# Kernel optimization log

Measured on AMD Instinct MI355X. Metric: run time of the kernel, lower is better.

## Reference

```python
import jax, jax.numpy as jnp
import numpy as np

N = 20000        # nodes
E = 320000       # edges (avg degree 16)
F_IN = 128       # node_features
F2 = 64          # second_features (per-head out dim, LSTM hidden)
H = 8            # heads
D1 = H * F2      # 512, concat output of GATConv / LSTM input
NEG_SLOPE = 0.2  # GATConv default leaky_relu slope


def _gat_conv(x, src, dst, W, att_src, att_dst, bias):
    """PyG GATConv (concat=True, self-loops added, eval-mode dropout)."""
    n = x.shape[0]
    h = (x @ W).reshape(n, H, -1)                      # [N,H,F]
    a_s = (h * att_src).sum(-1)                        # [N,H]
    a_d = (h * att_dst).sum(-1)                        # [N,H]
    e = jax.nn.leaky_relu(a_s[src] + a_d[dst], NEG_SLOPE)   # [E',H]
    m = jax.ops.segment_max(e, dst, num_segments=n)    # [N,H]
    m = jnp.where(jnp.isfinite(m), m, 0.0)
    ex = jnp.exp(e - m[dst])
    denom = jax.ops.segment_sum(ex, dst, num_segments=n)
    alpha = ex / (denom[dst] + 1e-16)                  # [E',H]
    msg = h[src] * alpha[:, :, None]                   # [E',H,F]
    out = jax.ops.segment_sum(msg, dst, num_segments=n)  # [N,H,F]
    return out.reshape(n, -1) + bias                   # [N,H*F]


def _lstm_step(x, W_ih, W_hh, b_ih, b_hh):
    """Single-timestep PyTorch LSTM with zero initial (h0, c0). x: [N,D1]."""
    h0 = jnp.zeros((x.shape[0], F2), x.dtype)
    gates = x @ W_ih.T + b_ih + h0 @ W_hh.T + b_hh     # [N,4*F2]
    i, f, g, o = jnp.split(gates, 4, axis=-1)
    c = jax.nn.sigmoid(f) * 0.0 + jax.nn.sigmoid(i) * jnp.tanh(g)
    h = jax.nn.sigmoid(o) * jnp.tanh(c)
    return h, (h, c)


def setup_inputs() -> dict:
    key = jax.random.key(0)
    ks = jax.random.split(key, 16)

    def glorot(k, shape, fan_in):
        return jax.random.normal(k, shape, jnp.float32) * (1.0 / np.sqrt(fan_in))

    return {
        "x": jax.random.normal(ks[0], (N, F_IN), jnp.float32),
        "edge_index": jax.random.randint(ks[1], (2, E), 0, N, jnp.int32),
        "edge_weight": jax.random.uniform(ks[2], (E,), jnp.float32),
        # GATConv 1: F_IN -> H*F2
        "W1": glorot(ks[3], (F_IN, H * F2), F_IN),
        "att_src1": glorot(ks[4], (H, F2), F2),
        "att_dst1": glorot(ks[5], (H, F2), F2),
        "bias1": jnp.zeros((H * F2,), jnp.float32),
        # LSTM: input D1 -> hidden F2
        "W_ih": glorot(ks[6], (4 * F2, D1), D1),
        "W_hh": glorot(ks[7], (4 * F2, F2), F2),
        "b_ih": jnp.zeros((4 * F2,), jnp.float32),
        "b_hh": jnp.zeros((4 * F2,), jnp.float32),
        # GATConv 2: F2 -> H*F2
        "W2": glorot(ks[8], (F2, H * F2), F2),
        "att_src2": glorot(ks[9], (H, F2), F2),
        "att_dst2": glorot(ks[10], (H, F2), F2),
        "bias2": jnp.zeros((H * F2,), jnp.float32),
    }


def reference(x, edge_index, edge_weight, W1, att_src1, att_dst1, bias1,
              W_ih, W_hh, b_ih, b_hh, W2, att_src2, att_dst2, bias2):
    # edge_weight is accepted but unused, matching the original forward.
    loops = jnp.arange(N, dtype=edge_index.dtype)
    src = jnp.concatenate([edge_index[0], loops])      # add self-loops (PyG default)
    dst = jnp.concatenate([edge_index[1], loops])

    h = _gat_conv(x, src, dst, W1, att_src1, att_dst1, bias1)   # [N,512]
    h, hidden2 = _lstm_step(h, W_ih, W_hh, b_ih, b_hh)          # [N,64]
    h = jax.nn.relu(h)
    h = _gat_conv(h, src, dst, W2, att_src2, att_dst2, bias2)   # [N,512]
    return jax.nn.softmax(h, axis=1)
```

## Files before the change

kernel.cpp:

```cpp
#include <hip/hip_runtime.h>
#include <math.h>
#include <stdint.h>


__global__ void count_kernel(const int* __restrict__ dst, int* __restrict__ deg, int E) {
  int i = blockIdx.x * 256 + threadIdx.x;
  if (i < E) atomicAdd(&deg[dst[i]], 1);
}

__global__ void scan_kernel(const int* __restrict__ deg, int* __restrict__ rowptr, int n) {
  __shared__ int buf[1024];
  const int tid = threadIdx.x;
  const int i0 = tid * 20;
  int v[20];
  int tsum = 0;
#pragma unroll
  for (int k = 0; k < 20; ++k) {
    int i = i0 + k;
    v[k] = (i < n) ? (deg[i] + 1) : 0;
    tsum += v[k];
  }
  int incl = tsum;
  buf[tid] = incl;
  __syncthreads();
  for (int s = 1; s < 1024; s <<= 1) {
    int t = (tid >= (unsigned)s) ? buf[tid - s] : 0;
    __syncthreads();
    incl += t;
    buf[tid] = incl;
    __syncthreads();
  }
  int excl = incl - tsum;
#pragma unroll
  for (int k = 0; k < 20; ++k) {
    int i = i0 + k;
    if (i < n) rowptr[i] = excl;
    excl += v[k];
  }
  if (tid == 1023) rowptr[n] = incl;
}

__global__ void scatter_kernel(const int* __restrict__ src, const int* __restrict__ dst,
                               const int* __restrict__ rowptr, int* __restrict__ wp,
                               int* __restrict__ col, int E, int n) {
  int i = blockIdx.x * 256 + threadIdx.x;
  if (i < E) {
    int d = dst[i];
    int p = rowptr[d] + atomicAdd(&wp[d], 1);
    col[p] = src[i];
  } else if (i < E + n) {
    int d = i - E;
    int p = rowptr[d] + atomicAdd(&wp[d], 1);
    col[p] = d;
  }
}


__device__ __forceinline__ uint16_t bf16r(float x) {
  uint32_t u = __float_as_uint(x);
  return (uint16_t)((u + 0x7FFFu + ((u >> 16) & 1u)) >> 16);
}
__device__ __forceinline__ void bfsplit(float x, uint16_t& h, uint16_t& l) {
  h = bf16r(x);
  float hf = __uint_as_float((uint32_t)h << 16);
  l = bf16r(x - hf);
}
__device__ __forceinline__ void store4split(uint16_t* oh, uint16_t* ol, float4 v) {
  ushort4 h, l;
  bfsplit(v.x, h.x, l.x); bfsplit(v.y, h.y, l.y);
  bfsplit(v.z, h.z, l.z); bfsplit(v.w, h.w, l.w);
  *reinterpret_cast<ushort4*>(oh) = h;
  *reinterpret_cast<ushort4*>(ol) = l;
}

__device__ __forceinline__ void gload16(const uint16_t* g, uint16_t* l) {
  __builtin_amdgcn_global_load_lds(
      (const __attribute__((address_space(1))) uint32_t*)g,
      (__attribute__((address_space(3))) uint32_t*)l, 16, 0, 0);
}

using bf16x8 = __attribute__((ext_vector_type(8))) short;
using f32x4  = __attribute__((ext_vector_type(4))) float;


template <bool SPLIT_OUT>
__global__ __launch_bounds__(256) void gemm_mfma(
    const uint16_t* __restrict__ Ah, const uint16_t* __restrict__ Al,
    const uint16_t* __restrict__ Bh, const uint16_t* __restrict__ Bl,
    float* __restrict__ C, uint16_t* __restrict__ Ch, uint16_t* __restrict__ Cl,
    const float* __restrict__ bias,
    int M, int K, int lda, int aZ, int bZ, int ldc, int cZ, int biasZ) {
  constexpr int BM = 64, BN = 64, BK = 64;
  constexpr int PL = BM * BK;
  __shared__ __align__(16) uint16_t sAh[2 * PL], sAl[2 * PL];
  __shared__ __align__(16) uint16_t sBh[2 * PL], sBl[2 * PL];
  const int z = blockIdx.z;
  Ah += (size_t)z * aZ; Al += (size_t)z * aZ;
  Bh += (size_t)z * bZ; Bl += (size_t)z * bZ;
  const int tid = threadIdx.x;
  const int wid = tid >> 6, lane = tid & 63;
  int L = blockIdx.x + gridDim.x * blockIdx.y;
  int nwg = gridDim.x * gridDim.y;
  int q = nwg >> 3, r = nwg & 7;
  int xcd = L & 7, gix = L >> 3;
  int base = (xcd < r) ? xcd * (q + 1) : r * (q + 1) + (xcd - r) * q;
  int w = base + gix;
  const int bm = (w / gridDim.x) * BM;
  const int bn = (w % gridDim.x) * BN;
  const int fr = lane & 15;
  const int kg = lane >> 4;
  const int mbase = wid * 16;
  f32x4 acc[4] = {};

  auto stage = [&](int sb, int k0) {
#pragma unroll
    for (int j = 0; j < 2; ++j) {
      int idx = (wid * 2 + j) * 64 + lane;
      int row = idx >> 3, c = idx & 7;
      int rg = min(bm + row, M - 1);
      size_t goA = (size_t)rg * lda + k0 + ((c ^ (row & 7)) << 3);
      uint16_t* ldst = sAh + sb * PL + (wid * 2 + j) * 512;
      gload16(Ah + goA, ldst);
      gload16(Al + goA, sAl + sb * PL + (wid * 2 + j) * 512);
      size_t goB = (size_t)(bn + row) * K + k0 + ((c ^ (row & 7)) << 3);
      gload16(Bh + goB, sBh + sb * PL + (wid * 2 + j) * 512);
      gload16(Bl + goB, sBl + sb * PL + (wid * 2 + j) * 512);
    }
  };

  stage(0, 0);
  __syncthreads();
  int buf = 0;
  for (int k0 = 0; k0 < K; k0 += BK) {
    const bool more = (k0 + BK) < K;
    if (more) stage(buf ^ 1, k0 + BK);
    const char* pAh = (const char*)sAh + buf * (PL * 2);
    const char* pAl = (const char*)sAl + buf * (PL * 2);
    const char* pBh = (const char*)sBh + buf * (PL * 2);
    const char* pBl = (const char*)sBl + buf * (PL * 2);
#pragma unroll
    for (int ks = 0; ks < 2; ++ks) {
      const int kc = ks * 4 + kg;
      bf16x8 ah, al, bh[4], bl[4];
      {
        int m = mbase + fr;
        int off = m * 128 + ((kc ^ (m & 7)) << 4);
        ah = *reinterpret_cast<const bf16x8*>(pAh + off);
        al = *reinterpret_cast<const bf16x8*>(pAl + off);
      }
#pragma unroll
      for (int j = 0; j < 4; ++j) {
        int n = j * 16 + fr;
        int off = n * 128 + ((kc ^ (n & 7)) << 4);
        bh[j] = *reinterpret_cast<const bf16x8*>(pBh + off);
        bl[j] = *reinterpret_cast<const bf16x8*>(pBl + off);
      }
#pragma unroll
      for (int j = 0; j < 4; ++j) {
        acc[j] = __builtin_amdgcn_mfma_f32_16x16x32_bf16(ah, bh[j], acc[j], 0, 0, 0);
        acc[j] = __builtin_amdgcn_mfma_f32_16x16x32_bf16(al, bh[j], acc[j], 0, 0, 0);
        acc[j] = __builtin_amdgcn_mfma_f32_16x16x32_bf16(ah, bl[j], acc[j], 0, 0, 0);
      }
    }
    if (more) {
      __syncthreads();
      buf ^= 1;
    }
  }
  float bz[4];
#pragma unroll
  for (int j = 0; j < 4; ++j)
    bz[j] = bias ? bias[(size_t)z * biasZ + bn + j * 16 + fr] : 0.f;
  if (SPLIT_OUT) {
    Ch += (size_t)z * cZ;
    Cl += (size_t)z * cZ;
  } else {
    C += (size_t)z * cZ;
  }
  {
    int mr = bm + mbase + kg * 4;
#pragma unroll
    for (int rr = 0; rr < 4; ++rr) {
      int m = mr + rr;
      if (m < M) {
#pragma unroll
        for (int j = 0; j < 4; ++j) {
          float v = acc[j][rr] + bz[j];
          size_t o = (size_t)m * ldc + bn + j * 16 + fr;
          if (SPLIT_OUT) {
            uint16_t h, l;
            bfsplit(v, h, l);
            Ch[o] = h; Cl[o] = l;
          } else {
            C[o] = v;
          }
        }
      }
    }
  }
}


__global__ void prep_all_kernel(const float* __restrict__ W_ih, const float* __restrict__ b_ih,
                                const float* __restrict__ b_hh, const float* __restrict__ W1,
                                const float* __restrict__ as1, const float* __restrict__ ad1,
                                const float* __restrict__ W2, const float* __restrict__ as2,
                                const float* __restrict__ ad2,
                                int* __restrict__ degwp,
                                uint16_t* __restrict__ Wtbh, uint16_t* __restrict__ Wtbl,
                                uint16_t* __restrict__ Bt1h, uint16_t* __restrict__ Bt1l,
                                uint16_t* __restrict__ Bt2h, uint16_t* __restrict__ Bt2l,
                                float* __restrict__ bsum, float* __restrict__ watt1,
                                float* __restrict__ watt2, int n2) {
  int idx = blockIdx.x * 256 + threadIdx.x;
  if (idx < n2) {
    degwp[idx] = 0;
    return;
  }
  int t = idx - n2;
  if (t < 98304) {
    int jp = t >> 9, k = t & 511;
    int j = (jp < 64) ? jp : jp + 64;
    uint16_t h, l;
    bfsplit(W_ih[(size_t)j * 512 + k], h, l);
    Wtbh[t] = h; Wtbl[t] = l;
    return;
  }
  t -= 98304;
  if (t < 65536) {
    int n = t >> 7, k = t & 127;
    uint16_t h, l;
    bfsplit(W1[(size_t)k * 512 + n], h, l);
    Bt1h[t] = h; Bt1l[t] = l;
    return;
  }
  t -= 65536;
  if (t < 32768) {
    int n = t >> 6, k = t & 63;
    uint16_t h, l;
    bfsplit(W2[(size_t)k * 512 + n], h, l);
    Bt2h[t] = h; Bt2l[t] = l;
    return;
  }
  t -= 32768;
  if (t < 192) {
    int j = (t < 64) ? t : t + 64;
    bsum[t] = b_ih[j] + b_hh[j];
    return;
  }
  t -= 192;
  if (t < 2048) {
    int f = t >> 4, c = t & 15;
    int k = c & 7;
    const float* att = ((c < 8) ? as1 : ad1) + k * 64;
    const float* w = W1 + (size_t)f * 512 + k * 64;
    float s = 0.f;
#pragma unroll
    for (int j = 0; j < 64; ++j) s = fmaf(w[j], att[j], s);
    watt1[t] = s;
    return;
  }
  t -= 2048;
  if (t < 1024) {
    int f = t >> 4, c = t & 15;
    int k = c & 7;
    const float* att = ((c < 8) ? as2 : ad2) + k * 64;
    const float* w = W2 + (size_t)f * 512 + k * 64;
    float s = 0.f;
#pragma unroll
    for (int j = 0; j < 64; ++j) s = fmaf(w[j], att[j], s);
    watt2[t] = s;
  }
}


template <int F>
__global__ __launch_bounds__(256) void attcoef_kernel(
    const float* __restrict__ feat, const float* __restrict__ watt,
    float* __restrict__ a_s, float* __restrict__ a_d, int n) {
  __shared__ float rows[16 * F];
  __shared__ float wbuf[F * 16];
  const int n0 = blockIdx.x * 16;
  const int tid = threadIdx.x;
  if (n0 + 16 <= n) {
    const float4* g = reinterpret_cast<const float4*>(feat + (size_t)n0 * F);
    float4* l = reinterpret_cast<float4*>(rows);
    for (int i = tid; i < 16 * F / 4; i += 256) l[i] = g[i];
  } else {
    for (int i = tid; i < 16 * F; i += 256) {
      int r = i / F;
      rows[i] = (n0 + r < n) ? feat[(size_t)(n0 + r) * F + (i - r * F)] : 0.f;
    }
  }
  {
    const float4* g = reinterpret_cast<const float4*>(watt);
    float4* l = reinterpret_cast<float4*>(wbuf);
    for (int i = tid; i < F * 16 / 4; i += 256) l[i] = g[i];
  }
  __syncthreads();
  const int local = tid >> 4, c = tid & 15;
  float s = 0.f;
#pragma unroll 8
  for (int f = 0; f < F; ++f) s = fmaf(rows[local * F + f], wbuf[f * 16 + c], s);
  const int node = n0 + local;
  if (node < n) {
    if (c < 8) a_s[(size_t)node * 8 + c] = s;
    else       a_d[(size_t)node * 8 + (c - 8)] = s;
  }
}


template <int F>
__global__ __launch_bounds__(256) void gat_aggregate_wave(
    const float* __restrict__ feat, const float* __restrict__ a_s,
    const float* __restrict__ a_d, const int* __restrict__ rowptr,
    const int* __restrict__ col, uint16_t* __restrict__ aggH,
    uint16_t* __restrict__ aggL, int n) {
  constexpr int FL = F / 4;
  constexpr int GROUPS = 64 / FL;
  constexpr int HPW = 8 / GROUPS;
  __shared__ float s_ex[4][8][8];
  __shared__ int s_cols[4][8];
  const int wid = threadIdx.x >> 6;
  const int lane = threadIdx.x & 63;
  const int node = blockIdx.x * 4 + wid;
  if (node >= n) return;
  const int start = rowptr[node];
  const int deg = rowptr[node + 1] - start;
  const int j = lane >> 3;
  const int h = lane & 7;
  const int grp = lane / FL;
  const int fl = lane % FL;
  const float adh = a_d[(size_t)node * 8 + h];
  float dpart = 0.f;
  float acc[8][4];
#pragma unroll
  for (int q = 0; q < 8; ++q)
#pragma unroll
    for (int t = 0; t < 4; ++t) acc[q][t] = 0.f;

  for (int c0 = 0; c0 < deg; c0 += 8) {
    float ex = 0.f;
    int sj = 0;
    if (c0 + j < deg) {
      sj = col[start + c0 + j];
      float v = a_s[(size_t)sj * 8 + h] + adh;
      v = (v > 0.f) ? v : 0.2f * v;
      ex = __expf(v);
    }
    s_ex[wid][j][h] = ex;
    if (h == 0) s_cols[wid][j] = sj;
    dpart += ex;
    __builtin_amdgcn_wave_barrier();
    const int ce = min(8, deg - c0);
    for (int e = grp; e < ce; e += GROUPS) {
      int s = s_cols[wid][e];
      float4 fv = *reinterpret_cast<const float4*>(feat + (size_t)s * F + fl * 4);
      float al[8];
      *reinterpret_cast<float4*>(&al[0]) = *reinterpret_cast<const float4*>(&s_ex[wid][e][0]);
      *reinterpret_cast<float4*>(&al[4]) = *reinterpret_cast<const float4*>(&s_ex[wid][e][4]);
#pragma unroll
      for (int q = 0; q < 8; ++q) {
        acc[q][0] = fmaf(al[q], fv.x, acc[q][0]);
        acc[q][1] = fmaf(al[q], fv.y, acc[q][1]);
        acc[q][2] = fmaf(al[q], fv.z, acc[q][2]);
        acc[q][3] = fmaf(al[q], fv.w, acc[q][3]);
      }
    }
    __builtin_amdgcn_wave_barrier();
  }
  dpart += __shfl_xor(dpart, 8);
  dpart += __shfl_xor(dpart, 16);
  dpart += __shfl_xor(dpart, 32);
#pragma unroll
  for (int q = 0; q < 8; ++q)
#pragma unroll
    for (int t = 0; t < 4; ++t) {
      float v = acc[q][t];
      if (GROUPS == 4) v += __shfl_xor(v, 16);
      v += __shfl_xor(v, 32);
      acc[q][t] = v;
    }
#pragma unroll
  for (int q = 0; q < 8; ++q) {
    float dq = __shfl(dpart, q);
    if (q / HPW == grp) {
      float dinv = 1.f / (dq + 1e-16f);
      size_t off = (size_t)node * 8 * F + (size_t)q * F + fl * 4;
      float4 o = make_float4(acc[q][0] * dinv, acc[q][1] * dinv,
                             acc[q][2] * dinv, acc[q][3] * dinv);
      store4split(aggH + off, aggL + off, o);
    }
  }
}


__global__ __launch_bounds__(256) void lstm_act_attcoef_kernel(
    const float* __restrict__ gates, const float* __restrict__ bsum,
    const float* __restrict__ watt2, float* __restrict__ h2,
    float* __restrict__ a_s2, float* __restrict__ a_d2, int n) {
  __shared__ float h2t[4][64];
  __shared__ float wbuf[64 * 16];
  const int tid = threadIdx.x;
  reinterpret_cast<float4*>(wbuf)[tid] = reinterpret_cast<const float4*>(watt2)[tid];
  const int nl = tid >> 6, j = tid & 63;
  const int node = blockIdx.x * 4 + nl;
  float hv = 0.f;
  if (node < n) {
    const float* g0 = gates + (size_t)node * 192;
    float iv = g0[j] + bsum[j];
    float gv = g0[64 + j] + bsum[64 + j];
    float ov = g0[128 + j] + bsum[128 + j];
    float c = (1.f / (1.f + __expf(-iv))) * tanhf(gv);
    hv = fmaxf((1.f / (1.f + __expf(-ov))) * tanhf(c), 0.f);
    h2[(size_t)node * 64 + j] = hv;
  }
  h2t[nl][j] = hv;
  __syncthreads();
  if (j < 16 && node < n) {
    float s = 0.f;
#pragma unroll 16
    for (int f = 0; f < 64; ++f) s = fmaf(h2t[nl][f], wbuf[f * 16 + j], s);
    if (j < 8) a_s2[(size_t)node * 8 + j] = s;
    else       a_d2[(size_t)node * 8 + (j - 8)] = s;
  }
}


__global__ __launch_bounds__(256) void softmax512_wave(const float* __restrict__ in,
                                                       float* __restrict__ out, int n) {
  const int wid = threadIdx.x >> 6, lane = threadIdx.x & 63;
  const int node = blockIdx.x * 4 + wid;
  if (node >= n) return;
  const float4* ip = reinterpret_cast<const float4*>(in + (size_t)node * 512);
  float4 v0 = ip[lane];
  float4 v1 = ip[64 + lane];
  float m = fmaxf(fmaxf(fmaxf(v0.x, v0.y), fmaxf(v0.z, v0.w)),
                  fmaxf(fmaxf(v1.x, v1.y), fmaxf(v1.z, v1.w)));
#pragma unroll
  for (int d = 1; d < 64; d <<= 1) m = fmaxf(m, __shfl_xor(m, d));
  float4 e0, e1;
  e0.x = __expf(v0.x - m); e0.y = __expf(v0.y - m);
  e0.z = __expf(v0.z - m); e0.w = __expf(v0.w - m);
  e1.x = __expf(v1.x - m); e1.y = __expf(v1.y - m);
  e1.z = __expf(v1.z - m); e1.w = __expf(v1.w - m);
  float s = e0.x + e0.y + e0.z + e0.w + e1.x + e1.y + e1.z + e1.w;
#pragma unroll
  for (int d = 1; d < 64; d <<= 1) s += __shfl_xor(s, d);
  float inv = 1.f / s;
  e0.x *= inv; e0.y *= inv; e0.z *= inv; e0.w *= inv;
  e1.x *= inv; e1.y *= inv; e1.z *= inv; e1.w *= inv;
  float4* op = reinterpret_cast<float4*>(out + (size_t)node * 512);
  op[lane] = e0;
  op[64 + lane] = e1;
}


extern "C" void kernel_launch(void* const* d_in, const int* in_sizes, int n_in,
                              void* d_out, int out_size, void* d_ws, size_t ws_size,
                              hipStream_t stream) {
  const float* x      = (const float*)d_in[0];
  const int*   ei     = (const int*)d_in[1];
  const float* W1     = (const float*)d_in[3];
  const float* att_s1 = (const float*)d_in[4];
  const float* att_d1 = (const float*)d_in[5];
  const float* bias1  = (const float*)d_in[6];
  const float* W_ih   = (const float*)d_in[7];
  const float* b_ih   = (const float*)d_in[9];
  const float* b_hh   = (const float*)d_in[10];
  const float* W2     = (const float*)d_in[11];
  const float* att_s2 = (const float*)d_in[12];
  const float* att_d2 = (const float*)d_in[13];
  const float* bias2  = (const float*)d_in[14];
  float* out = (float*)d_out;

  const int N = in_sizes[0] / 128;
  const int E = in_sizes[1] / 2;
  const int* src = ei;
  const int* dst = ei + E;

  char* p = (char*)d_ws;
  auto alloc = [&](size_t bytes) {
    char* r = p;
    p += (bytes + 255) & ~(size_t)255;
    return r;
  };
  char* slotA = alloc((size_t)N * 4096);
  char* slotB = alloc((size_t)N * 2048);
  float* a_s1 = (float*)alloc((size_t)N * 8 * 4);
  float* a_d1 = (float*)alloc((size_t)N * 8 * 4);
  float* a_s2 = (float*)alloc((size_t)N * 8 * 4);
  float* a_d2 = (float*)alloc((size_t)N * 8 * 4);
  float* watt1 = (float*)alloc(128 * 16 * 4);
  float* watt2 = (float*)alloc(64 * 16 * 4);
  uint16_t* Wtbh = (uint16_t*)alloc((size_t)192 * 512 * 2);
  uint16_t* Wtbl = (uint16_t*)alloc((size_t)192 * 512 * 2);
  uint16_t* Bt1h = (uint16_t*)alloc((size_t)512 * 128 * 2);
  uint16_t* Bt1l = (uint16_t*)alloc((size_t)512 * 128 * 2);
  uint16_t* Bt2h = (uint16_t*)alloc((size_t)512 * 64 * 2);
  uint16_t* Bt2l = (uint16_t*)alloc((size_t)512 * 64 * 2);
  float* bsum = (float*)alloc(192 * 4);
  int* deg    = (int*)alloc((size_t)2 * N * 4);
  int* wp     = deg + N;
  int* rowptr = (int*)alloc((size_t)(N + 1) * 4);
  int* col    = (int*)alloc((size_t)(E + N) * 4);

  uint16_t* agg1h = (uint16_t*)slotA;
  uint16_t* agg1l = agg1h + (size_t)N * 1024;
  float* gates2 = (float*)slotA;
  float* h2 = (float*)(slotA + (size_t)N * 768);
  uint16_t* agg2h = (uint16_t*)(slotA + (size_t)N * 1024);
  uint16_t* agg2l = agg2h + (size_t)N * 512;
  uint16_t* g1h = (uint16_t*)slotB;
  uint16_t* g1l = g1h + (size_t)N * 512;
  float* h3p = (float*)slotB;

  {
    int total = 2 * N + 98304 + 65536 + 32768 + 192 + 2048 + 1024;
    prep_all_kernel<<<(total + 255) / 256, 256, 0, stream>>>(
        W_ih, b_ih, b_hh, W1, att_s1, att_d1, W2, att_s2, att_d2,
        deg, Wtbh, Wtbl, Bt1h, Bt1l, Bt2h, Bt2l, bsum, watt1, watt2, 2 * N);
  }

  count_kernel<<<(E + 255) / 256, 256, 0, stream>>>(dst, deg, E);
  scan_kernel<<<1, 1024, 0, stream>>>(deg, rowptr, N);
  scatter_kernel<<<(E + N + 255) / 256, 256, 0, stream>>>(src, dst, rowptr, wp, col, E, N);

  const int NYB = (N + 63) / 64;

  attcoef_kernel<128><<<(N + 15) / 16, 256, 0, stream>>>(x, watt1, a_s1, a_d1, N);
  gat_aggregate_wave<128><<<(N + 3) / 4, 256, 0, stream>>>(x, a_s1, a_d1, rowptr, col,
                                                           agg1h, agg1l, N);
  {
    dim3 g(1, NYB, 8);
    gemm_mfma<true><<<g, 256, 0, stream>>>(
        agg1h, agg1l, Bt1h, Bt1l, nullptr, g1h, g1l, bias1,
        N, 128, 1024, 128, 64 * 128, 512, 64, 64);
  }

  {
    dim3 g(3, NYB, 1);
    gemm_mfma<false><<<g, 256, 0, stream>>>(
        g1h, g1l, Wtbh, Wtbl, gates2, nullptr, nullptr, nullptr,
        N, 512, 512, 0, 0, 192, 0, 0);
  }
  lstm_act_attcoef_kernel<<<(N + 3) / 4, 256, 0, stream>>>(gates2, bsum, watt2,
                                                           h2, a_s2, a_d2, N);

  gat_aggregate_wave<64><<<(N + 3) / 4, 256, 0, stream>>>(h2, a_s2, a_d2, rowptr, col,
                                                          agg2h, agg2l, N);
  {
    dim3 g(1, NYB, 8);
    gemm_mfma<false><<<g, 256, 0, stream>>>(
        agg2h, agg2l, Bt2h, Bt2l, h3p, nullptr, nullptr, bias2,
        N, 64, 512, 64, 64 * 64, 512, 64, 64);
  }
  softmax512_wave<<<(N + 3) / 4, 256, 0, stream>>>(h3p, out, N);
}
```

Baseline: 327.2 us.

## Repartition GAT aggregation lanes by head instead of by edge

The aggregation kernel now gives each lane group a subset of heads, not a subset of edges. Every lane walks all edges in the chunk and keeps only its HPW heads of accumulators. This removes the cross-lane shuffle reduction at the end and cuts accumulator registers from 32 to 4*HPW. Full chunks of 8 edges load all eight source-feature rows up front to raise memory-level parallelism. In exchange, each feature row is now loaded redundantly by several lane groups instead of once.

```diff
diff --git a/kernel.cpp b/kernel.cpp
--- a/kernel.cpp
+++ b/kernel.cpp
@@ -317,8 +317,7 @@
     const int* __restrict__ col, uint16_t* __restrict__ aggH,
     uint16_t* __restrict__ aggL, int n) {
   constexpr int FL = F / 4;
-  constexpr int GROUPS = 64 / FL;
-  constexpr int HPW = 8 / GROUPS;
+  constexpr int HPW = (F == 128) ? 4 : 2;
   __shared__ float s_ex[4][8][8];
   __shared__ int s_cols[4][8];
   const int wid = threadIdx.x >> 6;
@@ -329,15 +328,13 @@
   const int deg = rowptr[node + 1] - start;
   const int j = lane >> 3;
   const int h = lane & 7;
-  const int grp = lane / FL;
-  const int fl = lane % FL;
+  const int f4 = lane & (FL - 1);
+  const int hbase = (lane / FL) * HPW;
   const float adh = a_d[(size_t)node * 8 + h];
   float dpart = 0.f;
-  float acc[8][4];
-#pragma unroll
-  for (int q = 0; q < 8; ++q)
-#pragma unroll
-    for (int t = 0; t < 4; ++t) acc[q][t] = 0.f;
+  float4 acc[HPW];
+#pragma unroll
+  for (int q = 0; q < HPW; ++q) acc[q] = make_float4(0.f, 0.f, 0.f, 0.f);
 
   for (int c0 = 0; c0 < deg; c0 += 8) {
     float ex = 0.f;
@@ -352,19 +349,49 @@
     if (h == 0) s_cols[wid][j] = sj;
     dpart += ex;
     __builtin_amdgcn_wave_barrier();
-    const int ce = min(8, deg - c0);
-    for (int e = grp; e < ce; e += GROUPS) {
-      int s = s_cols[wid][e];
-      float4 fv = *reinterpret_cast<const float4*>(feat + (size_t)s * F + fl * 4);
-      float al[8];
-      *reinterpret_cast<float4*>(&al[0]) = *reinterpret_cast<const float4*>(&s_ex[wid][e][0]);
-      *reinterpret_cast<float4*>(&al[4]) = *reinterpret_cast<const float4*>(&s_ex[wid][e][4]);
-#pragma unroll
-      for (int q = 0; q < 8; ++q) {
-        acc[q][0] = fmaf(al[q], fv.x, acc[q][0]);
-        acc[q][1] = fmaf(al[q], fv.y, acc[q][1]);
-        acc[q][2] = fmaf(al[q], fv.z, acc[q][2]);
-        acc[q][3] = fmaf(al[q], fv.w, acc[q][3]);
+    if (deg - c0 >= 8) {
+      float4 fv[8];
+#pragma unroll
+      for (int e = 0; e < 8; ++e) {
+        int s = s_cols[wid][e];
+        fv[e] = *reinterpret_cast<const float4*>(feat + (size_t)s * F + f4 * 4);
+      }
+#pragma unroll
+      for (int e = 0; e < 8; ++e) {
+        float alv[HPW];
+        if constexpr (HPW == 4)
+          *reinterpret_cast<float4*>(alv) =
+              *reinterpret_cast<const float4*>(&s_ex[wid][e][hbase]);
+        else
+          *reinterpret_cast<float2*>(alv) =
+              *reinterpret_cast<const float2*>(&s_ex[wid][e][hbase]);
+#pragma unroll
+        for (int q = 0; q < HPW; ++q) {
+          acc[q].x = fmaf(alv[q], fv[e].x, acc[q].x);
+          acc[q].y = fmaf(alv[q], fv[e].y, acc[q].y);
+          acc[q].z = fmaf(alv[q], fv[e].z, acc[q].z);
+          acc[q].w = fmaf(alv[q], fv[e].w, acc[q].w);
+        }
+      }
+    } else {
+      const int ce = deg - c0;
+      for (int e = 0; e < ce; ++e) {
+        int s = s_cols[wid][e];
+        float4 fv = *reinterpret_cast<const float4*>(feat + (size_t)s * F + f4 * 4);
+        float alv[HPW];
+        if constexpr (HPW == 4)
+          *reinterpret_cast<float4*>(alv) =
+              *reinterpret_cast<const float4*>(&s_ex[wid][e][hbase]);
+        else
+          *reinterpret_cast<float2*>(alv) =
+              *reinterpret_cast<const float2*>(&s_ex[wid][e][hbase]);
+#pragma unroll
+        for (int q = 0; q < HPW; ++q) {
+          acc[q].x = fmaf(alv[q], fv.x, acc[q].x);
+          acc[q].y = fmaf(alv[q], fv.y, acc[q].y);
+          acc[q].z = fmaf(alv[q], fv.z, acc[q].z);
+          acc[q].w = fmaf(alv[q], fv.w, acc[q].w);
+        }
       }
     }
     __builtin_amdgcn_wave_barrier();
@@ -373,24 +400,13 @@
   dpart += __shfl_xor(dpart, 16);
   dpart += __shfl_xor(dpart, 32);
 #pragma unroll
-  for (int q = 0; q < 8; ++q)
-#pragma unroll
-    for (int t = 0; t < 4; ++t) {
-      float v = acc[q][t];
-      if (GROUPS == 4) v += __shfl_xor(v, 16);
-      v += __shfl_xor(v, 32);
-      acc[q][t] = v;
-    }
-#pragma unroll
-  for (int q = 0; q < 8; ++q) {
-    float dq = __shfl(dpart, q);
-    if (q / HPW == grp) {
-      float dinv = 1.f / (dq + 1e-16f);
-      size_t off = (size_t)node * 8 * F + (size_t)q * F + fl * 4;
-      float4 o = make_float4(acc[q][0] * dinv, acc[q][1] * dinv,
-                             acc[q][2] * dinv, acc[q][3] * dinv);
-      store4split(aggH + off, aggL + off, o);
-    }
+  for (int q = 0; q < HPW; ++q) {
+    float dq = __shfl(dpart, hbase + q);
+    float dinv = 1.f / (dq + 1e-16f);
+    size_t off = (size_t)node * 8 * F + (size_t)(hbase + q) * F + f4 * 4;
+    float4 o = make_float4(acc[q].x * dinv, acc[q].y * dinv,
+                           acc[q].z * dinv, acc[q].w * dinv);
+    store4split(aggH + off, aggL + off, o);
   }
 }
 
```

New measurement: 321.0 us. About the same (-1.9%).
